# Kernel tuning notes

Hardware: AMD Instinct MI355X
Metric: run time of the kernel (lower is better)

The kernel has to match this reference:

```python
import jax, jax.numpy as jnp
import numpy as np

N_NODES = 200000
D_IN = 256
D_OUT = 256
B = 4096
K1 = 25   # layer-1 fanout
K2 = 10   # layer-2 fanout
M = B * (1 + K2)  # layer-1 node set size: batch centers + their sampled neighbors


def setup_inputs() -> dict:
    key = jax.random.key(0)
    k1, k2, k3, k4, k5, k6 = jax.random.split(key, 6)
    features = jax.random.normal(k1, (N_NODES, D_IN), dtype=jnp.float32)
    # SageLayer weights: [out, 2*in] (concat path, gcn=False); small kaiming-like scale
    W1 = jax.random.normal(k2, (D_OUT, 2 * D_IN), dtype=jnp.float32) * 0.05
    W2 = jax.random.normal(k3, (D_OUT, 2 * D_OUT), dtype=jnp.float32) * 0.05
    nodes_batch = jax.random.randint(k4, (B,), 0, N_NODES, dtype=jnp.int64)
    neigh2 = jax.random.randint(k5, (B, K2), 0, N_NODES, dtype=jnp.int64)
    neigh1 = jax.random.randint(k6, (M, K1), 0, N_NODES, dtype=jnp.int64)
    return {"features": features, "W1": W1, "W2": W2,
            "nodes_batch": nodes_batch, "neigh2": neigh2, "neigh1": neigh1}


def reference(features, W1, W2, nodes_batch, neigh2, neigh1):
    # Layer-1 node set: centers first, then their sampled layer-2 neighbors.
    l1_nodes = jnp.concatenate([nodes_batch, neigh2.reshape(-1)])  # [M]
    # ---- layer 1: MEAN aggregate over K1 sampled neighbors (gather + mean) ----
    agg1 = jnp.mean(features[neigh1], axis=1)          # [M, K1, D_IN] -> [M, D_IN]
    self1 = features[l1_nodes]                         # [M, D_IN]
    # SageLayer: relu(W.mm(cat(self, agg).T)).T == relu(cat @ W.T)
    h1 = jax.nn.relu(jnp.concatenate([self1, agg1], axis=1) @ W1.T)  # [M, D_OUT]
    # ---- layer 2: centers are h1[:B]; neighbor embeddings are h1[B:] in blocks of K2 ----
    nb = nodes_batch.shape[0]
    agg2 = jnp.mean(h1[nb:].reshape(nb, -1, h1.shape[1]), axis=1)    # [B, D_OUT]
    h2 = jax.nn.relu(jnp.concatenate([h1[:nb], agg2], axis=1) @ W2.T)  # [B, D_OUT]
    return h2
```

## Files before the change

kernel.cpp:

```cpp
#include <hip/hip_runtime.h>
#include <hip/hip_bf16.h>

typedef __attribute__((ext_vector_type(8))) short bf16x8;
typedef __attribute__((ext_vector_type(4))) float f32x4;
typedef __attribute__((ext_vector_type(2))) float f32x2;

#define B_SZ   4096
#define K1     25
#define K2     10
#define M_L1   45056
#define D      256
#define K_DIM  512
#define N_NODES 200000

static __device__ __forceinline__ unsigned short f2bf(float f) {
    union { float f; unsigned u; } v; v.f = f;
    return (unsigned short)((v.u + 0x7fffu + ((v.u >> 16) & 1u)) >> 16);
}
static __device__ __forceinline__ float bf2f(unsigned short h) {
    union { unsigned u; float f; } v; v.u = ((unsigned)h) << 16;
    return v.f;
}

__global__ __launch_bounds__(256)
void convert_fp8(const float* __restrict__ f, unsigned* __restrict__ f8) {
    const size_t i = ((size_t)blockIdx.x * 256 + threadIdx.x) * 8;
    const float4 a = *(const float4*)(f + i);
    const float4 b = *(const float4*)(f + i + 4);
    unsigned u0 = 0, u1 = 0;
    u0 = __builtin_amdgcn_cvt_pk_fp8_f32(a.x, a.y, u0, false);
    u0 = __builtin_amdgcn_cvt_pk_fp8_f32(a.z, a.w, u0, true);
    u1 = __builtin_amdgcn_cvt_pk_fp8_f32(b.x, b.y, u1, false);
    u1 = __builtin_amdgcn_cvt_pk_fp8_f32(b.z, b.w, u1, true);
    uint2 r; r.x = u0; r.y = u1;
    *(uint2*)(f8 + (i >> 2)) = r;
}

__global__ __launch_bounds__(256)
void convert_w(const float* __restrict__ W1, const float* __restrict__ W2,
               unsigned short* __restrict__ W1b, unsigned short* __restrict__ W2b) {
    const int i = blockIdx.x * 256 + threadIdx.x;
    W1b[i] = f2bf(W1[i]);
    W2b[i] = f2bf(W2[i]);
}

__global__ __launch_bounds__(256)
void fused_l1(const float* __restrict__ feat,
              const unsigned* __restrict__ f8,
              const int* __restrict__ nodes_batch,
              const int* __restrict__ neigh2,
              const int* __restrict__ neigh1,
              const unsigned short* __restrict__ W1b,
              unsigned short* __restrict__ h1) {
    __shared__ unsigned short At[64 * 512];
    const int tid  = threadIdx.x;
    const int w    = tid >> 6, lane = tid & 63;
    const int quad = lane >> 4, l16 = lane & 15;
    const int row0 = blockIdx.x << 6;

    for (int t = 0; t < 16; ++t) {
        const int r = (w << 4) + t;
        const int m = row0 + r;
        const int self_node = (m < B_SZ) ? nodes_batch[m] : neigh2[m - B_SZ];
        const int* nb = neigh1 + (size_t)m * K1;
        int idxv = (lane < K1) ? nb[lane] : 0;
        const float4 s = *(const float4*)(feat + (size_t)self_node * D + (lane << 2));
        unsigned q[K1];
        #pragma unroll
        for (int j = 0; j < K1; ++j)
            q[j] = f8[(size_t)__shfl(idxv, j) * (D / 4) + lane];
        float a0 = 0.f, a1 = 0.f, a2 = 0.f, a3 = 0.f;
        #pragma unroll
        for (int j = 0; j < K1; ++j) {
            const f32x2 lo = __builtin_amdgcn_cvt_pk_f32_fp8(q[j], false);
            const f32x2 hi = __builtin_amdgcn_cvt_pk_f32_fp8(q[j], true);
            a0 += lo.x; a1 += lo.y; a2 += hi.x; a3 += hi.y;
        }
        const float inv = 1.0f / (float)K1;
        const int cs = lane >> 1;
        const int ca = 32 + cs;
        const int slotS = (cs & 56) | ((cs ^ r) & 7);
        const int slotA = (ca & 56) | ((ca ^ r) & 7);
        const int sub = (lane & 1) << 2;
        *(ushort4*)&At[r * 512 + slotS * 8 + sub] =
            make_ushort4(f2bf(s.x), f2bf(s.y), f2bf(s.z), f2bf(s.w));
        *(ushort4*)&At[r * 512 + slotA * 8 + sub] =
            make_ushort4(f2bf(a0 * inv), f2bf(a1 * inv), f2bf(a2 * inv), f2bf(a3 * inv));
    }
    __syncthreads();

    const int wn = w << 6;
    f32x4 acc[4][4];
    #pragma unroll
    for (int i = 0; i < 4; ++i)
        #pragma unroll
        for (int j = 0; j < 4; ++j)
            acc[i][j] = (f32x4){0.f, 0.f, 0.f, 0.f};

    #pragma unroll 4
    for (int s = 0; s < 16; ++s) {
        bf16x8 bfr[4], af[4];
        #pragma unroll
        for (int ni = 0; ni < 4; ++ni)
            bfr[ni] = *(const bf16x8*)(W1b +
                (size_t)(wn + ni * 16 + l16) * K_DIM + s * 32 + quad * 8);
        #pragma unroll
        for (int mi = 0; mi < 4; ++mi) {
            const int rr = mi * 16 + l16;
            const int c = (s << 2) + quad;
            const int slot = (c & 56) | ((c ^ rr) & 7);
            af[mi] = *(const bf16x8*)&At[rr * 512 + slot * 8];
        }
        #pragma unroll
        for (int mi = 0; mi < 4; ++mi)
            #pragma unroll
            for (int ni = 0; ni < 4; ++ni)
                acc[mi][ni] = __builtin_amdgcn_mfma_f32_16x16x32_bf16(
                    af[mi], bfr[ni], acc[mi][ni], 0, 0, 0);
    }

    #pragma unroll
    for (int mi = 0; mi < 4; ++mi)
        #pragma unroll
        for (int ni = 0; ni < 4; ++ni)
            #pragma unroll
            for (int r = 0; r < 4; ++r) {
                const size_t gm = (size_t)row0 + mi * 16 + quad * 4 + r;
                const size_t gn = wn + ni * 16 + l16;
                float v = acc[mi][ni][r];
                h1[gm * D + gn] = f2bf(v > 0.f ? v : 0.f);
            }
}

__global__ __launch_bounds__(256)
void agg2_kernel(const unsigned short* __restrict__ h1,
                 unsigned short* __restrict__ X2) {
    const int wave = threadIdx.x >> 6;
    const int lane = threadIdx.x & 63;
    const int b = (blockIdx.x << 2) + wave;
    const ushort4 s = *(const ushort4*)(h1 + (size_t)b * D + (lane << 2));
    float sx = 0.f, sy = 0.f, sz = 0.f, sw = 0.f;
    #pragma unroll
    for (int k = 0; k < K2; ++k) {
        const ushort4 v = *(const ushort4*)(h1 + (size_t)(B_SZ + b * K2 + k) * D + (lane << 2));
        sx += bf2f(v.x); sy += bf2f(v.y); sz += bf2f(v.z); sw += bf2f(v.w);
    }
    const float inv = 1.0f / (float)K2;
    unsigned short* xr = X2 + (size_t)b * K_DIM;
    *(ushort4*)(xr + (lane << 2)) = s;
    *(ushort4*)(xr + D + (lane << 2)) =
        make_ushort4(f2bf(sx * inv), f2bf(sy * inv), f2bf(sz * inv), f2bf(sw * inv));
}

template<bool OUT_BF16>
__global__ __launch_bounds__(256)
void gemm_relu(const unsigned short* __restrict__ A,
               const unsigned short* __restrict__ W,
               void* __restrict__ Cout) {
    __shared__ unsigned short As[128 * 64];
    __shared__ unsigned short Bs[128 * 64];
    const int tid  = threadIdx.x;
    const int w    = tid >> 6, lane = tid & 63;
    const int quad = lane >> 4, l16 = lane & 15;
    const int wm = (w >> 1) << 6;
    const int wn = (w & 1) << 6;
    const size_t row0 = (size_t)blockIdx.x * 128;
    const size_t col0 = (size_t)blockIdx.y * 128;

    const int srow   = (w << 5) + (lane >> 3);
    const int schunk = ((lane & 7) ^ (lane >> 3)) << 3;
    const unsigned short* aG = A + (row0 + srow) * K_DIM + schunk;
    const unsigned short* bG = W + (col0 + srow) * K_DIM + schunk;

    f32x4 acc[4][4];
    #pragma unroll
    for (int i = 0; i < 4; ++i)
        #pragma unroll
        for (int j = 0; j < 4; ++j)
            acc[i][j] = (f32x4){0.f, 0.f, 0.f, 0.f};

    for (int k0 = 0; k0 < K_DIM; k0 += 64) {
        __syncthreads();
        #pragma unroll
        for (int n = 0; n < 4; ++n) {
            __builtin_amdgcn_global_load_lds(
                (const __attribute__((address_space(1))) void*)(aG + (size_t)(n * 8) * K_DIM + k0),
                (__attribute__((address_space(3))) void*)(As + ((w << 2) + n) * 512),
                16, 0, 0);
            __builtin_amdgcn_global_load_lds(
                (const __attribute__((address_space(1))) void*)(bG + (size_t)(n * 8) * K_DIM + k0),
                (__attribute__((address_space(3))) void*)(Bs + ((w << 2) + n) * 512),
                16, 0, 0);
        }
        __syncthreads();
        #pragma unroll
        for (int ks = 0; ks < 2; ++ks) {
            bf16x8 af[4], bfr[4];
            #pragma unroll
            for (int i = 0; i < 4; ++i) {
                const int row = wm + i * 16 + l16;
                af[i] = *(const bf16x8*)&As[row * 64 + ((((ks << 2) + quad) ^ (l16 & 7)) << 3)];
            }
            #pragma unroll
            for (int i = 0; i < 4; ++i) {
                const int row = wn + i * 16 + l16;
                bfr[i] = *(const bf16x8*)&Bs[row * 64 + ((((ks << 2) + quad) ^ (l16 & 7)) << 3)];
            }
            #pragma unroll
            for (int mi = 0; mi < 4; ++mi)
                #pragma unroll
                for (int ni = 0; ni < 4; ++ni)
                    acc[mi][ni] = __builtin_amdgcn_mfma_f32_16x16x32_bf16(
                        af[mi], bfr[ni], acc[mi][ni], 0, 0, 0);
        }
    }

    #pragma unroll
    for (int mi = 0; mi < 4; ++mi) {
        #pragma unroll
        for (int ni = 0; ni < 4; ++ni) {
            #pragma unroll
            for (int r = 0; r < 4; ++r) {
                const size_t gm = row0 + wm + mi * 16 + quad * 4 + r;
                const size_t gn = col0 + wn + ni * 16 + l16;
                float v = acc[mi][ni][r];
                v = v > 0.f ? v : 0.f;
                if (OUT_BF16)
                    ((unsigned short*)Cout)[gm * D + gn] = f2bf(v);
                else
                    ((float*)Cout)[gm * D + gn] = v;
            }
        }
    }
}

extern "C" void kernel_launch(void* const* d_in, const int* in_sizes, int n_in,
                              void* d_out, int out_size, void* d_ws, size_t ws_size,
                              hipStream_t stream) {
    const float* feat        = (const float*)d_in[0];
    const float* W1          = (const float*)d_in[1];
    const float* W2          = (const float*)d_in[2];
    const int*   nodes_batch = (const int*)d_in[3];
    const int*   neigh2      = (const int*)d_in[4];
    const int*   neigh1      = (const int*)d_in[5];
    float* out = (float*)d_out;

    char* ws = (char*)d_ws;
    unsigned*       f8   = (unsigned*)(ws);
    unsigned short* h1   = (unsigned short*)(ws + 51200000);
    unsigned short* X2   = (unsigned short*)(ws + 51200000 + 23068672);
    unsigned short* W1b  = (unsigned short*)(ws + 51200000 + 23068672 + 4194304);
    unsigned short* W2b  = (unsigned short*)(ws + 51200000 + 23068672 + 4194304 + 262144);

    convert_fp8<<<25000, 256, 0, stream>>>(feat, f8);
    convert_w<<<512, 256, 0, stream>>>(W1, W2, W1b, W2b);
    fused_l1<<<M_L1 / 64, 256, 0, stream>>>(feat, f8, nodes_batch, neigh2, neigh1, W1b, h1);
    agg2_kernel<<<B_SZ / 4, 256, 0, stream>>>(h1, X2);
    gemm_relu<false><<<dim3(B_SZ / 128, 2), 256, 0, stream>>>(X2, W2b, out);
}
```

Measured before the change: 386.3 us.

## Halve fused layer-1 tile to 32 rows, prefetch neighbor indices, merge conversion kernels

Merges the feature fp8 conversion and weight bf16 conversion into one launch. The fused layer-1 gather+GEMM kernel now handles 32 rows per block instead of 64, halving its LDS tile and doubling the grid to 1408 blocks, so more blocks can be resident and the gather latency is better hidden. Each wave now loads all eight rows' neighbor indices up front instead of one row at a time. The trade-off is that every block re-reads the full W1 from global/L2, so twice as many blocks each load the whole weight, and fewer MFMAs are done per B-fragment load.

```diff
diff --git a/kernel.cpp b/kernel.cpp
--- a/kernel.cpp
+++ b/kernel.cpp
@@ -23,25 +23,26 @@
 }
 
 __global__ __launch_bounds__(256)
-void convert_fp8(const float* __restrict__ f, unsigned* __restrict__ f8) {
-    const size_t i = ((size_t)blockIdx.x * 256 + threadIdx.x) * 8;
-    const float4 a = *(const float4*)(f + i);
-    const float4 b = *(const float4*)(f + i + 4);
-    unsigned u0 = 0, u1 = 0;
-    u0 = __builtin_amdgcn_cvt_pk_fp8_f32(a.x, a.y, u0, false);
-    u0 = __builtin_amdgcn_cvt_pk_fp8_f32(a.z, a.w, u0, true);
-    u1 = __builtin_amdgcn_cvt_pk_fp8_f32(b.x, b.y, u1, false);
-    u1 = __builtin_amdgcn_cvt_pk_fp8_f32(b.z, b.w, u1, true);
-    uint2 r; r.x = u0; r.y = u1;
-    *(uint2*)(f8 + (i >> 2)) = r;
-}
-
-__global__ __launch_bounds__(256)
-void convert_w(const float* __restrict__ W1, const float* __restrict__ W2,
-               unsigned short* __restrict__ W1b, unsigned short* __restrict__ W2b) {
-    const int i = blockIdx.x * 256 + threadIdx.x;
-    W1b[i] = f2bf(W1[i]);
-    W2b[i] = f2bf(W2[i]);
+void convert_all(const float* __restrict__ f, unsigned* __restrict__ f8,
+                 const float* __restrict__ W1, const float* __restrict__ W2,
+                 unsigned short* __restrict__ W1b, unsigned short* __restrict__ W2b) {
+    const int bid = blockIdx.x;
+    if (bid < 25000) {
+        const size_t i = ((size_t)bid * 256 + threadIdx.x) * 8;
+        const float4 a = *(const float4*)(f + i);
+        const float4 b = *(const float4*)(f + i + 4);
+        unsigned u0 = 0, u1 = 0;
+        u0 = __builtin_amdgcn_cvt_pk_fp8_f32(a.x, a.y, u0, false);
+        u0 = __builtin_amdgcn_cvt_pk_fp8_f32(a.z, a.w, u0, true);
+        u1 = __builtin_amdgcn_cvt_pk_fp8_f32(b.x, b.y, u1, false);
+        u1 = __builtin_amdgcn_cvt_pk_fp8_f32(b.z, b.w, u1, true);
+        uint2 r; r.x = u0; r.y = u1;
+        *(uint2*)(f8 + (i >> 2)) = r;
+    } else {
+        const int i = (bid - 25000) * 256 + threadIdx.x;
+        W1b[i] = f2bf(W1[i]);
+        W2b[i] = f2bf(W2[i]);
+    }
 }
 
 __global__ __launch_bounds__(256)
@@ -52,23 +53,27 @@
               const int* __restrict__ neigh1,
               const unsigned short* __restrict__ W1b,
               unsigned short* __restrict__ h1) {
-    __shared__ unsigned short At[64 * 512];
+    __shared__ unsigned short At[32 * 512];
     const int tid  = threadIdx.x;
     const int w    = tid >> 6, lane = tid & 63;
     const int quad = lane >> 4, l16 = lane & 15;
-    const int row0 = blockIdx.x << 6;
-
-    for (int t = 0; t < 16; ++t) {
-        const int r = (w << 4) + t;
+    const int row0 = blockIdx.x << 5;
+
+    const int* nbBase = neigh1 + (size_t)(row0 + (w << 3)) * K1;
+    int idxs[8];
+    #pragma unroll
+    for (int t = 0; t < 8; ++t)
+        idxs[t] = (lane < K1) ? nbBase[t * K1 + lane] : 0;
+
+    for (int t = 0; t < 8; ++t) {
+        const int r = (w << 3) + t;
         const int m = row0 + r;
         const int self_node = (m < B_SZ) ? nodes_batch[m] : neigh2[m - B_SZ];
-        const int* nb = neigh1 + (size_t)m * K1;
-        int idxv = (lane < K1) ? nb[lane] : 0;
         const float4 s = *(const float4*)(feat + (size_t)self_node * D + (lane << 2));
         unsigned q[K1];
         #pragma unroll
         for (int j = 0; j < K1; ++j)
-            q[j] = f8[(size_t)__shfl(idxv, j) * (D / 4) + lane];
+            q[j] = f8[(size_t)__shfl(idxs[t], j) * (D / 4) + lane];
         float a0 = 0.f, a1 = 0.f, a2 = 0.f, a3 = 0.f;
         #pragma unroll
         for (int j = 0; j < K1; ++j) {
@@ -90,29 +95,29 @@
     __syncthreads();
 
     const int wn = w << 6;
-    f32x4 acc[4][4];
-    #pragma unroll
-    for (int i = 0; i < 4; ++i)
+    f32x4 acc[2][4];
+    #pragma unroll
+    for (int i = 0; i < 2; ++i)
         #pragma unroll
         for (int j = 0; j < 4; ++j)
             acc[i][j] = (f32x4){0.f, 0.f, 0.f, 0.f};
 
     #pragma unroll 4
     for (int s = 0; s < 16; ++s) {
-        bf16x8 bfr[4], af[4];
+        bf16x8 bfr[4], af[2];
         #pragma unroll
         for (int ni = 0; ni < 4; ++ni)
             bfr[ni] = *(const bf16x8*)(W1b +
                 (size_t)(wn + ni * 16 + l16) * K_DIM + s * 32 + quad * 8);
         #pragma unroll
-        for (int mi = 0; mi < 4; ++mi) {
+        for (int mi = 0; mi < 2; ++mi) {
             const int rr = mi * 16 + l16;
             const int c = (s << 2) + quad;
             const int slot = (c & 56) | ((c ^ rr) & 7);
             af[mi] = *(const bf16x8*)&At[rr * 512 + slot * 8];
         }
         #pragma unroll
-        for (int mi = 0; mi < 4; ++mi)
+        for (int mi = 0; mi < 2; ++mi)
             #pragma unroll
             for (int ni = 0; ni < 4; ++ni)
                 acc[mi][ni] = __builtin_amdgcn_mfma_f32_16x16x32_bf16(
@@ -120,7 +125,7 @@
     }
 
     #pragma unroll
-    for (int mi = 0; mi < 4; ++mi)
+    for (int mi = 0; mi < 2; ++mi)
         #pragma unroll
         for (int ni = 0; ni < 4; ++ni)
             #pragma unroll
@@ -152,11 +157,10 @@
         make_ushort4(f2bf(sx * inv), f2bf(sy * inv), f2bf(sz * inv), f2bf(sw * inv));
 }
 
-template<bool OUT_BF16>
 __global__ __launch_bounds__(256)
 void gemm_relu(const unsigned short* __restrict__ A,
                const unsigned short* __restrict__ W,
-               void* __restrict__ Cout) {
+               float* __restrict__ Cout) {
     __shared__ unsigned short As[128 * 64];
     __shared__ unsigned short Bs[128 * 64];
     const int tid  = threadIdx.x;
@@ -216,22 +220,16 @@
     }
 
     #pragma unroll
-    for (int mi = 0; mi < 4; ++mi) {
-        #pragma unroll
-        for (int ni = 0; ni < 4; ++ni) {
+    for (int mi = 0; mi < 4; ++mi)
+        #pragma unroll
+        for (int ni = 0; ni < 4; ++ni)
             #pragma unroll
             for (int r = 0; r < 4; ++r) {
                 const size_t gm = row0 + wm + mi * 16 + quad * 4 + r;
                 const size_t gn = col0 + wn + ni * 16 + l16;
                 float v = acc[mi][ni][r];
-                v = v > 0.f ? v : 0.f;
-                if (OUT_BF16)
-                    ((unsigned short*)Cout)[gm * D + gn] = f2bf(v);
-                else
-                    ((float*)Cout)[gm * D + gn] = v;
-            }
-        }
-    }
+                Cout[gm * D + gn] = v > 0.f ? v : 0.f;
+            }
 }
 
 extern "C" void kernel_launch(void* const* d_in, const int* in_sizes, int n_in,
@@ -252,9 +250,8 @@
     unsigned short* W1b  = (unsigned short*)(ws + 51200000 + 23068672 + 4194304);
     unsigned short* W2b  = (unsigned short*)(ws + 51200000 + 23068672 + 4194304 + 262144);
 
-    convert_fp8<<<25000, 256, 0, stream>>>(feat, f8);
-    convert_w<<<512, 256, 0, stream>>>(W1, W2, W1b, W2b);
-    fused_l1<<<M_L1 / 64, 256, 0, stream>>>(feat, f8, nodes_batch, neigh2, neigh1, W1b, h1);
+    convert_all<<<25512, 256, 0, stream>>>(feat, f8, W1, W2, W1b, W2b);
+    fused_l1<<<M_L1 / 32, 256, 0, stream>>>(feat, f8, nodes_batch, neigh2, neigh1, W1b, h1);
     agg2_kernel<<<B_SZ / 4, 256, 0, stream>>>(h1, X2);
-    gemm_relu<false><<<dim3(B_SZ / 128, 2), 256, 0, stream>>>(X2, W2b, out);
-}
+    gemm_relu<<<dim3(B_SZ / 128, 2), 256, 0, stream>>>(X2, W2b, out);
+}
```

Result: no change. 392.2 us (+1.5%).
